# Kernel tuning notes

Measured on AMD Instinct MI355X. Metric: run time of the kernel, lower is better.

## Reference

```python
import jax, jax.numpy as jnp
import numpy as np

T_EPS = 1e-07
NUM_CAPSULE = 10
DIM_CAPSULE = 64
ROUTINGS = 5


def squash(x, axis=-1):
    # NOTE: this repo's 'squash' is just norm-division (no s/(1+s) factor)
    s = jnp.sum(x * x, axis=axis, keepdims=True)
    return x / jnp.sqrt(s + T_EPS)


def setup_inputs() -> dict:
    key = jax.random.key(0)
    k1, k2 = jax.random.split(key)
    B, N, D = 128, 512, 300
    M = NUM_CAPSULE * DIM_CAPSULE  # 640
    x = jax.random.normal(k1, (B, N, D), dtype=jnp.float32)
    # xavier_normal for shape (1, D, M): std = sqrt(2/(fan_in+fan_out))
    std = float(np.sqrt(2.0 / (D + M)))
    W = jax.random.normal(k2, (1, D, M), dtype=jnp.float32) * std
    return {"x": x, "W": W}


def reference(x, W):
    B, N, D = x.shape
    # u_hat_vecs: [B, num_capsule(i), input_num_capsule(j), dim_capsule(k)]
    u = jnp.einsum('bnd,dm->bnm', x, W[0])
    u = u.reshape(B, N, NUM_CAPSULE, DIM_CAPSULE).transpose(0, 2, 1, 3)
    b = jnp.zeros((B, NUM_CAPSULE, N), dtype=x.dtype)
    outputs = None
    for i in range(ROUTINGS):
        # softmax over the num_capsule axis (axis=1 of b), matching the
        # permute(0,2,1) -> softmax(dim=2) -> permute back in torch
        c = jax.nn.softmax(b, axis=1)
        outputs = squash(jnp.einsum('bij,bijk->bik', c, u))  # [B, num, dim]
        if i < ROUTINGS - 1:
            b = jnp.einsum('bik,bijk->bij', outputs, u)
    return outputs
```

## Files before the change

### kernel.cpp

```cpp
#include <hip/hip_runtime.h>
#include <hip/hip_bf16.h>
#include <stdint.h>

#define BQ 128
#define NJ 512
#define DD 300
#define NC 10
#define DC 64
#define MM 640
#define KP 320
#define RT 5

typedef __attribute__((ext_vector_type(8))) short short8;
typedef __attribute__((ext_vector_type(4))) float f32x4;


__global__ void k_cast_x(const float* __restrict__ x, __hip_bfloat16* __restrict__ xb) {
    int g = blockIdx.x * 256 + threadIdx.x;
    int row = g / 40, cg = g - row * 40;
    const float* src = x + (size_t)row * DD + cg * 8;
    float4 a = make_float4(0.f, 0.f, 0.f, 0.f), b4 = a;
    if (cg < 37) { a = *(const float4*)src; b4 = *(const float4*)(src + 4); }
    else if (cg == 37) { a = *(const float4*)src; }
    union { ushort u[8]; uint4 v; } o;
    float f[8] = {a.x, a.y, a.z, a.w, b4.x, b4.y, b4.z, b4.w};
#pragma unroll
    for (int e = 0; e < 8; ++e) {
        __hip_bfloat16 h = __float2bfloat16(f[e]);
        o.u[e] = *(ushort*)&h;
    }
    *(uint4*)(xb + (size_t)row * KP + cg * 8) = o.v;
}

__global__ void k_cast_w(const float* __restrict__ w, __hip_bfloat16* __restrict__ wt) {
    int idx = blockIdx.x * 256 + threadIdx.x;
    int m = idx / KP, k = idx - m * KP;
    float v = (k < DD) ? w[(size_t)k * MM + m] : 0.f;
    wt[idx] = __float2bfloat16(v);
}


__global__ __launch_bounds__(256)
void k_gemm(const __hip_bfloat16* __restrict__ A,
            const __hip_bfloat16* __restrict__ Bt,
            __hip_bfloat16* __restrict__ C) {
    __shared__ __align__(16) __hip_bfloat16 As[128 * 64];
    __shared__ __align__(16) __hip_bfloat16 Bs[128 * 64];

    const int L  = blockIdx.x;
    const int n0 = ((L >> 3) % 5) * 128;
    const int m0 = ((L / 40) * 8 + (L & 7)) * 128;
    const int t  = threadIdx.x;
    const int w  = t >> 6, lane = t & 63;
    const int wrow = (w >> 1) * 64, wcol = (w & 1) * 64;
    const int quad = lane >> 4, r = lane & 15;

    f32x4 acc[4][4] = {};

    const int srow = t >> 3;
    const int sl   = (t & 7) ^ (srow & 7);
    const __hip_bfloat16* ag = A  + (size_t)(m0 + srow) * KP + sl * 8;
    const __hip_bfloat16* bg = Bt + (size_t)(n0 + srow) * KP + sl * 8;

    for (int kt = 0; kt < KP / 64; ++kt) {
        __syncthreads();
#pragma unroll
        for (int s = 0; s < 4; ++s) {
            __builtin_amdgcn_global_load_lds(
                (const __attribute__((address_space(1))) void*)(ag + (size_t)s * 32 * KP + kt * 64),
                (__attribute__((address_space(3))) void*)(&As[s * 2048 + t * 8]), 16, 0, 0);
            __builtin_amdgcn_global_load_lds(
                (const __attribute__((address_space(1))) void*)(bg + (size_t)s * 32 * KP + kt * 64),
                (__attribute__((address_space(3))) void*)(&Bs[s * 2048 + t * 8]), 16, 0, 0);
        }
        __syncthreads();

#pragma unroll
        for (int h = 0; h < 2; ++h) {
            short8 af[4], bf[4];
#pragma unroll
            for (int mi = 0; mi < 4; ++mi) {
                int rho = wrow + mi * 16 + r;
                int p = (h * 4 + quad) ^ (rho & 7);
                af[mi] = *(const short8*)&As[rho * 64 + p * 8];
            }
#pragma unroll
            for (int ni = 0; ni < 4; ++ni) {
                int rho = wcol + ni * 16 + r;
                int p = (h * 4 + quad) ^ (rho & 7);
                bf[ni] = *(const short8*)&Bs[rho * 64 + p * 8];
            }
#pragma unroll
            for (int mi = 0; mi < 4; ++mi)
#pragma unroll
                for (int ni = 0; ni < 4; ++ni)
                    acc[mi][ni] = __builtin_amdgcn_mfma_f32_16x16x32_bf16(
                        af[mi], bf[ni], acc[mi][ni], 0, 0, 0);
        }
    }

#pragma unroll
    for (int mi = 0; mi < 4; ++mi) {
#pragma unroll
        for (int ni = 0; ni < 4; ++ni) {
            int col = n0 + wcol + ni * 16 + r;
#pragma unroll
            for (int p = 0; p < 4; ++p) {
                int row = m0 + wrow + mi * 16 + quad * 4 + p;
                C[(size_t)row * MM + col] = __float2bfloat16(acc[mi][ni][p]);
            }
        }
    }
}


#define TJ 16
#define NT 8
#define TILE_BYTES (TJ * MM * 2)

__global__ __launch_bounds__(512)
void k_pass(const __hip_bfloat16* __restrict__ u, const float* __restrict__ pprev,
            float* __restrict__ pnext, int it) {
    __shared__ __align__(16) char smem[TILE_BYTES + 32 * 161 * 4 + 160 * 4 + MM * 4];
    ushort* ub    = (ushort*)smem;
    float*  red   = (float*)(smem + TILE_BYTES);
    float*  blj   = (float*)(smem + TILE_BYTES + 20608);
    float*  outl  = (float*)(smem + TILE_BYTES + 20608 + 640);
    float*  pored = (float*)smem;

    const int t   = threadIdx.x;
    const int blk = blockIdx.x;
    const int b   = blk >> 2, q = blk & 3;
    const int w   = t >> 6, lane = t & 63;
    const int jd  = t >> 5, kg = t & 31;

    const char* ubase = (const char*)(u + (size_t)(b * NJ + q * 128) * MM);

    uint4 sa = *(const uint4*)(ubase + t * 16);
    uint4 sb = *(const uint4*)(ubase + 8192 + t * 16);
    uint2 sc = *(const uint2*)(ubase + 16384 + t * 8);

    if (it > 0 && w < 5) {
        const float* pp = pprev + (size_t)b * 4 * MM;
        float s0 = 0.f, s1 = 0.f;
#pragma unroll
        for (int qq = 0; qq < 4; ++qq) {
            s0 += pp[qq * MM + w * 64 + lane];
            s1 += pp[qq * MM + 320 + w * 64 + lane];
        }
        float q0 = s0 * s0, q1 = s1 * s1;
#pragma unroll
        for (int m = 32; m >= 1; m >>= 1) {
            q0 += __shfl_xor(q0, m, 64);
            q1 += __shfl_xor(q1, m, 64);
        }
        outl[w * 64 + lane]       = s0 * rsqrtf(q0 + 1e-7f);
        outl[320 + w * 64 + lane] = s1 * rsqrtf(q1 + 1e-7f);
    }

    float po[20];
#pragma unroll
    for (int e = 0; e < 20; ++e) po[e] = 0.f;

    for (int tt = 0; tt < NT; ++tt) {
        uint4 na, nb; uint2 nc2;
        if (tt + 1 < NT) {
            const char* ns = ubase + (size_t)(tt + 1) * TILE_BYTES;
            na  = *(const uint4*)(ns + t * 16);
            nb  = *(const uint4*)(ns + 8192 + t * 16);
            nc2 = *(const uint2*)(ns + 16384 + t * 8);
        }
        __syncthreads();
        *(uint4*)((char*)ub + t * 16)        = sa;
        *(uint4*)((char*)ub + 8192 + t * 16) = sb;
        *(uint2*)((char*)ub + 16384 + t * 8) = sc;
        __syncthreads();

        const ushort* urow = ub + jd * MM;
        uint uv[10];
#pragma unroll
        for (int i = 0; i < 10; ++i)
            uv[i] = *(const uint*)(urow + i * 64 + kg * 2);

        float c[10];
        if (it > 0) {
#pragma unroll
            for (int i = 0; i < 10; ++i) {
                float u0 = __uint_as_float(uv[i] << 16);
                float u1 = __uint_as_float(uv[i] & 0xffff0000u);
                float2 oo = *(const float2*)(outl + i * 64 + kg * 2);
                red[kg * 161 + jd * 10 + i] = u0 * oo.x + u1 * oo.y;
            }
            __syncthreads();
            if (t < 160) {
                float s = 0.f;
#pragma unroll
                for (int g = 0; g < 32; ++g) s += red[g * 161 + t];
                blj[t] = s;
            }
            __syncthreads();
            float bl[10], mx = -1e30f;
#pragma unroll
            for (int i = 0; i < 10; ++i) { bl[i] = blj[jd * 10 + i]; mx = fmaxf(mx, bl[i]); }
            float ssum = 0.f;
#pragma unroll
            for (int i = 0; i < 10; ++i) { bl[i] = __expf(bl[i] - mx); ssum += bl[i]; }
            float inv = 1.f / ssum;
#pragma unroll
            for (int i = 0; i < 10; ++i) c[i] = bl[i] * inv;
        } else {
#pragma unroll
            for (int i = 0; i < 10; ++i) c[i] = 0.1f;
        }
#pragma unroll
        for (int i = 0; i < 10; ++i) {
            float u0 = __uint_as_float(uv[i] << 16);
            float u1 = __uint_as_float(uv[i] & 0xffff0000u);
            po[i * 2 + 0] += c[i] * u0;
            po[i * 2 + 1] += c[i] * u1;
        }
        sa = na; sb = nb; sc = nc2;
    }

#pragma unroll
    for (int e = 0; e < 20; ++e) po[e] += __shfl_xor(po[e], 32, 64);
    __syncthreads();
    if ((t & 63) < 32) {
#pragma unroll
        for (int e = 0; e < 20; ++e) pored[(w * 32 + kg) * 20 + e] = po[e];
    }
    __syncthreads();
    for (int m = t; m < MM; m += 512) {
        int i = m >> 6, k = m & 63, kg2 = k >> 1, kd = k & 1;
        float s = 0.f;
#pragma unroll
        for (int ww = 0; ww < 8; ++ww) s += pored[(ww * 32 + kg2) * 20 + i * 2 + kd];
        pnext[(size_t)blk * MM + m] = s;
    }
}

__global__ __launch_bounds__(640)
void k_squash(const float* __restrict__ pbuf, float* __restrict__ dst) {
    int b = blockIdx.x, t = threadIdx.x;
    float s = 0.f;
#pragma unroll
    for (int qq = 0; qq < 4; ++qq) s += pbuf[(size_t)(b * 4 + qq) * MM + t];
    float sq = s * s;
#pragma unroll
    for (int m = 32; m >= 1; m >>= 1) sq += __shfl_xor(sq, m, 64);
    dst[(size_t)b * MM + t] = s * rsqrtf(sq + 1e-7f);
}


extern "C" void kernel_launch(void* const* d_in, const int* in_sizes, int n_in,
                              void* d_out, int out_size, void* d_ws, size_t ws_size,
                              hipStream_t stream) {
    const float* x = (const float*)d_in[0];
    const float* W = (const float*)d_in[1];
    float* out = (float*)d_out;

    char* ws = (char*)d_ws;
    size_t o = 0;
    __hip_bfloat16* xb = (__hip_bfloat16*)(ws + o); o += (size_t)BQ * NJ * KP * 2;
    __hip_bfloat16* wt = (__hip_bfloat16*)(ws + o); o += (size_t)MM * KP * 2;
    __hip_bfloat16* u  = (__hip_bfloat16*)(ws + o); o += (size_t)BQ * NJ * MM * 2;
    float* pb0 = (float*)(ws + o); o += (size_t)512 * MM * 4;
    float* pb1 = (float*)(ws + o); o += (size_t)512 * MM * 4;

    k_cast_x<<<(BQ * NJ * 40) / 256, 256, 0, stream>>>(x, xb);
    k_cast_w<<<(MM * KP) / 256, 256, 0, stream>>>(W, wt);
    k_gemm<<<2560, 256, 0, stream>>>(xb, wt, u);

    float* pb[2] = {pb0, pb1};
    for (int t = 0; t < RT; ++t)
        k_pass<<<512, 512, 0, stream>>>(u, pb[(t + 1) & 1], pb[t & 1], t);
    k_squash<<<BQ, 640, 0, stream>>>(pb[(RT - 1) & 1], out);
}
```

Baseline: 256.1 us.

## Fuse first routing pass into GEMM epilogue via column-sum atomics

The GEMM epilogue now reduces each output column over its 128 rows and atomically adds the result into a per-batch sum buffer, which is zeroed beforehand. With uniform coupling 0.1, this gives the first routing iteration's output directly, so one full pass over the u tensor is dropped (four k_pass launches instead of five). It adds a small zero kernel and atomics in the GEMM, and sums fp32 accumulators rather than bf16-rounded values, which slightly changes numerics.

```diff
diff --git a/kernel.cpp b/kernel.cpp
--- a/kernel.cpp
+++ b/kernel.cpp
@@ -17,19 +17,19 @@
 
 __global__ void k_cast_x(const float* __restrict__ x, __hip_bfloat16* __restrict__ xb) {
     int g = blockIdx.x * 256 + threadIdx.x;
-    int row = g / 40, cg = g - row * 40;
-    const float* src = x + (size_t)row * DD + cg * 8;
+    int row = g / 40, cg2 = g - row * 40;
+    const float* src = x + (size_t)row * DD + cg2 * 8;
     float4 a = make_float4(0.f, 0.f, 0.f, 0.f), b4 = a;
-    if (cg < 37) { a = *(const float4*)src; b4 = *(const float4*)(src + 4); }
-    else if (cg == 37) { a = *(const float4*)src; }
+    if (cg2 < 37) { a = *(const float4*)src; b4 = *(const float4*)(src + 4); }
+    else if (cg2 == 37) { a = *(const float4*)src; }
     union { ushort u[8]; uint4 v; } o;
     float f[8] = {a.x, a.y, a.z, a.w, b4.x, b4.y, b4.z, b4.w};
 #pragma unroll
     for (int e = 0; e < 8; ++e) {
-        __hip_bfloat16 h = __float2bfloat16(f[e]);
-        o.u[e] = *(ushort*)&h;
-    }
-    *(uint4*)(xb + (size_t)row * KP + cg * 8) = o.v;
+        __hip_bfloat16 hh = __float2bfloat16(f[e]);
+        o.u[e] = *(ushort*)&hh;
+    }
+    *(uint4*)(xb + (size_t)row * KP + cg2 * 8) = o.v;
 }
 
 __global__ void k_cast_w(const float* __restrict__ w, __hip_bfloat16* __restrict__ wt) {
@@ -39,11 +39,16 @@
     wt[idx] = __float2bfloat16(v);
 }
 
+__global__ void k_zero(float4* __restrict__ p) {
+    p[blockIdx.x * 256 + threadIdx.x] = make_float4(0.f, 0.f, 0.f, 0.f);
+}
+
 
 __global__ __launch_bounds__(256)
 void k_gemm(const __hip_bfloat16* __restrict__ A,
             const __hip_bfloat16* __restrict__ Bt,
-            __hip_bfloat16* __restrict__ C) {
+            __hip_bfloat16* __restrict__ C,
+            float* __restrict__ su) {
     __shared__ __align__(16) __hip_bfloat16 As[128 * 64];
     __shared__ __align__(16) __hip_bfloat16 Bs[128 * 64];
 
@@ -76,18 +81,18 @@
         __syncthreads();
 
 #pragma unroll
-        for (int h = 0; h < 2; ++h) {
+        for (int hh = 0; hh < 2; ++hh) {
             short8 af[4], bf[4];
 #pragma unroll
             for (int mi = 0; mi < 4; ++mi) {
                 int rho = wrow + mi * 16 + r;
-                int p = (h * 4 + quad) ^ (rho & 7);
+                int p = (hh * 4 + quad) ^ (rho & 7);
                 af[mi] = *(const short8*)&As[rho * 64 + p * 8];
             }
 #pragma unroll
             for (int ni = 0; ni < 4; ++ni) {
                 int rho = wcol + ni * 16 + r;
-                int p = (h * 4 + quad) ^ (rho & 7);
+                int p = (hh * 4 + quad) ^ (rho & 7);
                 bf[ni] = *(const short8*)&Bs[rho * 64 + p * 8];
             }
 #pragma unroll
@@ -100,7 +105,7 @@
     }
 
 #pragma unroll
-    for (int mi = 0; mi < 4; ++mi) {
+    for (int mi = 0; mi < 4; ++mi)
 #pragma unroll
         for (int ni = 0; ni < 4; ++ni) {
             int col = n0 + wcol + ni * 16 + r;
@@ -110,6 +115,24 @@
                 C[(size_t)row * MM + col] = __float2bfloat16(acc[mi][ni][p]);
             }
         }
+
+    float cs[4];
+#pragma unroll
+    for (int ni = 0; ni < 4; ++ni) {
+        float s = 0.f;
+#pragma unroll
+        for (int mi = 0; mi < 4; ++mi)
+#pragma unroll
+            for (int p = 0; p < 4; ++p) s += acc[mi][ni][p];
+        s += __shfl_xor(s, 16, 64);
+        s += __shfl_xor(s, 32, 64);
+        cs[ni] = s;
+    }
+    if (quad == 0) {
+        int bb = m0 >> 9;
+#pragma unroll
+        for (int ni = 0; ni < 4; ++ni)
+            atomicAdd(&su[(size_t)bb * MM + n0 + wcol + ni * 16 + r], cs[ni]);
     }
 }
 
@@ -120,7 +143,7 @@
 
 __global__ __launch_bounds__(512)
 void k_pass(const __hip_bfloat16* __restrict__ u, const float* __restrict__ pprev,
-            float* __restrict__ pnext, int it) {
+            float* __restrict__ pnext, int first) {
     __shared__ __align__(16) char smem[TILE_BYTES + 32 * 161 * 4 + 160 * 4 + MM * 4];
     ushort* ub    = (ushort*)smem;
     float*  red   = (float*)(smem + TILE_BYTES);
@@ -140,13 +163,19 @@
     uint4 sb = *(const uint4*)(ubase + 8192 + t * 16);
     uint2 sc = *(const uint2*)(ubase + 16384 + t * 8);
 
-    if (it > 0 && w < 5) {
-        const float* pp = pprev + (size_t)b * 4 * MM;
-        float s0 = 0.f, s1 = 0.f;
-#pragma unroll
-        for (int qq = 0; qq < 4; ++qq) {
-            s0 += pp[qq * MM + w * 64 + lane];
-            s1 += pp[qq * MM + 320 + w * 64 + lane];
+    if (w < 5) {
+        float s0, s1;
+        if (first) {
+            s0 = 0.1f * pprev[(size_t)b * MM + w * 64 + lane];
+            s1 = 0.1f * pprev[(size_t)b * MM + 320 + w * 64 + lane];
+        } else {
+            const float* pp = pprev + (size_t)b * 4 * MM;
+            s0 = 0.f; s1 = 0.f;
+#pragma unroll
+            for (int qq = 0; qq < 4; ++qq) {
+                s0 += pp[qq * MM + w * 64 + lane];
+                s1 += pp[qq * MM + 320 + w * 64 + lane];
+            }
         }
         float q0 = s0 * s0, q1 = s1 * s1;
 #pragma unroll
@@ -157,6 +186,12 @@
         outl[w * 64 + lane]       = s0 * rsqrtf(q0 + 1e-7f);
         outl[320 + w * 64 + lane] = s1 * rsqrtf(q1 + 1e-7f);
     }
+    __syncthreads();
+
+    float2 oreg[10];
+#pragma unroll
+    for (int i = 0; i < 10; ++i)
+        oreg[i] = *(const float2*)&outl[i * 64 + kg * 2];
 
     float po[20];
 #pragma unroll
@@ -182,23 +217,22 @@
         for (int i = 0; i < 10; ++i)
             uv[i] = *(const uint*)(urow + i * 64 + kg * 2);
 
+#pragma unroll
+        for (int i = 0; i < 10; ++i) {
+            float u0 = __uint_as_float(uv[i] << 16);
+            float u1 = __uint_as_float(uv[i] & 0xffff0000u);
+            red[kg * 161 + jd * 10 + i] = u0 * oreg[i].x + u1 * oreg[i].y;
+        }
+        __syncthreads();
+        if (t < 160) {
+            float s = 0.f;
+#pragma unroll
+            for (int g = 0; g < 32; ++g) s += red[g * 161 + t];
+            blj[t] = s;
+        }
+        __syncthreads();
         float c[10];
-        if (it > 0) {
-#pragma unroll
-            for (int i = 0; i < 10; ++i) {
-                float u0 = __uint_as_float(uv[i] << 16);
-                float u1 = __uint_as_float(uv[i] & 0xffff0000u);
-                float2 oo = *(const float2*)(outl + i * 64 + kg * 2);
-                red[kg * 161 + jd * 10 + i] = u0 * oo.x + u1 * oo.y;
-            }
-            __syncthreads();
-            if (t < 160) {
-                float s = 0.f;
-#pragma unroll
-                for (int g = 0; g < 32; ++g) s += red[g * 161 + t];
-                blj[t] = s;
-            }
-            __syncthreads();
+        {
             float bl[10], mx = -1e30f;
 #pragma unroll
             for (int i = 0; i < 10; ++i) { bl[i] = blj[jd * 10 + i]; mx = fmaxf(mx, bl[i]); }
@@ -208,9 +242,6 @@
             float inv = 1.f / ssum;
 #pragma unroll
             for (int i = 0; i < 10; ++i) c[i] = bl[i] * inv;
-        } else {
-#pragma unroll
-            for (int i = 0; i < 10; ++i) c[i] = 0.1f;
         }
 #pragma unroll
         for (int i = 0; i < 10; ++i) {
@@ -266,13 +297,16 @@
     __hip_bfloat16* u  = (__hip_bfloat16*)(ws + o); o += (size_t)BQ * NJ * MM * 2;
     float* pb0 = (float*)(ws + o); o += (size_t)512 * MM * 4;
     float* pb1 = (float*)(ws + o); o += (size_t)512 * MM * 4;
+    float* su  = (float*)(ws + o); o += (size_t)BQ * MM * 4;
 
     k_cast_x<<<(BQ * NJ * 40) / 256, 256, 0, stream>>>(x, xb);
     k_cast_w<<<(MM * KP) / 256, 256, 0, stream>>>(W, wt);
-    k_gemm<<<2560, 256, 0, stream>>>(xb, wt, u);
-
-    float* pb[2] = {pb0, pb1};
-    for (int t = 0; t < RT; ++t)
-        k_pass<<<512, 512, 0, stream>>>(u, pb[(t + 1) & 1], pb[t & 1], t);
-    k_squash<<<BQ, 640, 0, stream>>>(pb[(RT - 1) & 1], out);
-}
+    k_zero<<<(BQ * MM) / (4 * 256), 256, 0, stream>>>((float4*)su);
+    k_gemm<<<2560, 256, 0, stream>>>(xb, wt, u, su);
+
+    k_pass<<<512, 512, 0, stream>>>(u, su,  pb0, 1);
+    k_pass<<<512, 512, 0, stream>>>(u, pb0, pb1, 0);
+    k_pass<<<512, 512, 0, stream>>>(u, pb1, pb0, 0);
+    k_pass<<<512, 512, 0, stream>>>(u, pb0, pb1, 0);
+    k_squash<<<BQ, 640, 0, stream>>>(pb1, out);
+}
```

Result: slower. 287.8 us (+12.3%).
